# Optimization experiments

Hardware: AMD Instinct MI355X
Metric: run time of the kernel (lower is better)

## Reference

```python
import jax, jax.numpy as jnp
import numpy as np

B, T, S, H, K, NQ = 16, 512, 320, 512, 1024, 4


def setup_inputs() -> dict:
    key = jax.random.key(0)
    ks = jax.random.split(key, 16)
    inp = {
        "waveform": jax.random.normal(ks[0], (B, T * S), dtype=jnp.float32) * 0.1,
        # Encoder: Linear(S->H) + LayerNorm(H)
        "enc_w": jax.random.normal(ks[1], (S, H), dtype=jnp.float32) * 0.02,
        "enc_b": jnp.zeros((H,), dtype=jnp.float32),
        "ln_g": jnp.ones((H,), dtype=jnp.float32),
        "ln_b": jnp.zeros((H,), dtype=jnp.float32),
        # Residual VQ codebooks: (NQ, K, H)
        "codebooks": jax.random.normal(ks[2], (NQ, K, H), dtype=jnp.float32) * 0.5,
        # 2-layer LSTM (torch gate order i,f,g,o), stacked over layers
        "lstm_wi": jax.random.normal(ks[3], (2, 4 * H, H), dtype=jnp.float32) * 0.04,
        "lstm_wh": jax.random.normal(ks[4], (2, 4 * H, H), dtype=jnp.float32) * 0.04,
        "lstm_bi": jnp.zeros((2, 4 * H), dtype=jnp.float32),
        "lstm_bh": jnp.zeros((2, 4 * H), dtype=jnp.float32),
        # Decoder out projection: Linear(H->S)
        "dec_w": jax.random.normal(ks[5], (H, S), dtype=jnp.float32) * 0.02,
        "dec_b": jnp.zeros((S,), dtype=jnp.float32),
    }
    return inp


def _layer_norm(x, g, b, eps=1e-5):
    mu = jnp.mean(x, axis=-1, keepdims=True)
    var = jnp.mean((x - mu) ** 2, axis=-1, keepdims=True)
    return (x - mu) * jax.lax.rsqrt(var + eps) * g + b


def _lstm_layer(x, wi, wh, bi, bh):
    # x: (B, T, H) -> (B, T, H); torch gate order i, f, g, o
    h0 = jnp.zeros((x.shape[0], wh.shape[1]), dtype=x.dtype)
    c0 = jnp.zeros_like(h0)

    def step(carry, xt):
        h, c = carry
        gates = xt @ wi.T + h @ wh.T + bi + bh  # (B, 4H)
        i, f, g, o = jnp.split(gates, 4, axis=-1)
        c = jax.nn.sigmoid(f) * c + jax.nn.sigmoid(i) * jnp.tanh(g)
        h = jax.nn.sigmoid(o) * jnp.tanh(c)
        return (h, c), h

    _, ys = jax.lax.scan(step, (h0, c0), x.transpose(1, 0, 2))
    return ys.transpose(1, 0, 2)


def reference(waveform, enc_w, enc_b, ln_g, ln_b, codebooks,
              lstm_wi, lstm_wh, lstm_bi, lstm_bh, dec_w, dec_b):
    # Encoder: unflatten to frames, project, LayerNorm, ReLU -> (B, T, H)
    x = waveform.reshape(B, T, S) @ enc_w + enc_b
    x = jax.nn.relu(_layer_norm(x, ln_g, ln_b))

    # Residual VQ (encodec-style): nearest-neighbor + straight-through estimator
    residual = x
    quant_out = jnp.zeros_like(x)
    losses = []
    for q in range(NQ):
        E = codebooks[q]  # (K, H)
        # squared L2 distance: ||r||^2 - 2 r.E^T + ||E||^2  -> (B, T, K)
        d = (jnp.sum(residual ** 2, axis=-1, keepdims=True)
             - 2.0 * jnp.einsum("bth,kh->btk", residual, E)
             + jnp.sum(E ** 2, axis=-1))
        idx = jnp.argmin(d, axis=-1)  # (B, T)
        quantized = E[idx]  # (B, T, H)
        losses.append(jnp.mean((jax.lax.stop_gradient(quantized) - residual) ** 2))
        q_st = residual + jax.lax.stop_gradient(quantized - residual)  # STE
        quant_out = quant_out + q_st
        residual = residual - q_st
    codebook_loss = jnp.stack(losses)  # (NQ,)

    # Decoder: 2-layer LSTM + out projection, flatten frames back to samples
    h = _lstm_layer(quant_out, lstm_wi[0], lstm_wh[0], lstm_bi[0], lstm_bh[0])
    h = _lstm_layer(h, lstm_wi[1], lstm_wh[1], lstm_bi[1], lstm_bh[1])
    out = h @ dec_w + dec_b  # (B, T, S)
    recon = out.reshape(B, T * S)
    return recon, codebook_loss
```

## Files before the change

### kernel.cpp

```cpp
#include <hip/hip_runtime.h>
#include <cmath>


template<bool BT>
__global__ __launch_bounds__(256)
void gemm64(const float* __restrict__ A, const float* __restrict__ B,
            float* __restrict__ C, int M, int N, int K,
            const float* __restrict__ bias1, const float* __restrict__ bias2)
{
    __shared__ float Al[32][68];
    __shared__ float Bl[32][68];
    const int m0 = blockIdx.y * 64, n0 = blockIdx.x * 64;
    const int t = threadIdx.x;
    const int tm = t >> 4, tn = t & 15;
    float acc[4][4] = {{0.f, 0.f, 0.f, 0.f}};

    for (int k0 = 0; k0 < K; k0 += 32) {
        #pragma unroll
        for (int i = 0; i < 2; i++) {
            int f4 = t + i * 256;
            int row = f4 >> 3, c4 = f4 & 7;
            float4 v = *(const float4*)(A + (size_t)(m0 + row) * K + k0 + c4 * 4);
            Al[c4*4+0][row] = v.x; Al[c4*4+1][row] = v.y;
            Al[c4*4+2][row] = v.z; Al[c4*4+3][row] = v.w;
        }
        if (BT) {
            #pragma unroll
            for (int i = 0; i < 2; i++) {
                int f4 = t + i * 256;
                int row = f4 >> 3, c4 = f4 & 7;
                float4 v = *(const float4*)(B + (size_t)(n0 + row) * K + k0 + c4 * 4);
                Bl[c4*4+0][row] = v.x; Bl[c4*4+1][row] = v.y;
                Bl[c4*4+2][row] = v.z; Bl[c4*4+3][row] = v.w;
            }
        } else {
            #pragma unroll
            for (int i = 0; i < 2; i++) {
                int f4 = t + i * 256;
                int kk = f4 >> 4, c4 = f4 & 15;
                float4 v = *(const float4*)(B + (size_t)(k0 + kk) * N + n0 + c4 * 4);
                *(float4*)&Bl[kk][c4 * 4] = v;
            }
        }
        __syncthreads();
        #pragma unroll
        for (int k = 0; k < 32; k++) {
            float4 a4 = *(const float4*)&Al[k][tm * 4];
            float4 b4 = *(const float4*)&Bl[k][tn * 4];
            float av[4] = {a4.x, a4.y, a4.z, a4.w};
            float bv[4] = {b4.x, b4.y, b4.z, b4.w};
            #pragma unroll
            for (int i = 0; i < 4; i++)
                #pragma unroll
                for (int j = 0; j < 4; j++)
                    acc[i][j] = fmaf(av[i], bv[j], acc[i][j]);
        }
        __syncthreads();
    }
    float bn[4];
    #pragma unroll
    for (int j = 0; j < 4; j++) {
        float bb = 0.f;
        if (bias1) bb += bias1[n0 + tn * 4 + j];
        if (bias2) bb += bias2[n0 + tn * 4 + j];
        bn[j] = bb;
    }
    #pragma unroll
    for (int i = 0; i < 4; i++) {
        float4 o;
        o.x = acc[i][0] + bn[0]; o.y = acc[i][1] + bn[1];
        o.z = acc[i][2] + bn[2]; o.w = acc[i][3] + bn[3];
        *(float4*)(C + (size_t)(m0 + tm * 4 + i) * N + n0 + tn * 4) = o;
    }
}

template<bool BT>
__global__ __launch_bounds__(256)
void gemm128(const float* __restrict__ A, const float* __restrict__ B,
             float* __restrict__ C, int M, int N, int K,
             const float* __restrict__ bias1, const float* __restrict__ bias2)
{
    __shared__ float Al[16][132];
    __shared__ float Bl[16][132];
    const int m0 = blockIdx.y * 128, n0 = blockIdx.x * 128;
    const int t = threadIdx.x;
    const int tm = t >> 4, tn = t & 15;
    float acc[8][8] = {};

    for (int k0 = 0; k0 < K; k0 += 16) {
        #pragma unroll
        for (int i = 0; i < 2; i++) {
            int f4 = t + i * 256;
            int row = f4 >> 2, c4 = f4 & 3;
            float4 v = *(const float4*)(A + (size_t)(m0 + row) * K + k0 + c4 * 4);
            Al[c4*4+0][row] = v.x; Al[c4*4+1][row] = v.y;
            Al[c4*4+2][row] = v.z; Al[c4*4+3][row] = v.w;
        }
        if (BT) {
            #pragma unroll
            for (int i = 0; i < 2; i++) {
                int f4 = t + i * 256;
                int row = f4 >> 2, c4 = f4 & 3;
                float4 v = *(const float4*)(B + (size_t)(n0 + row) * K + k0 + c4 * 4);
                Bl[c4*4+0][row] = v.x; Bl[c4*4+1][row] = v.y;
                Bl[c4*4+2][row] = v.z; Bl[c4*4+3][row] = v.w;
            }
        } else {
            #pragma unroll
            for (int i = 0; i < 2; i++) {
                int f4 = t + i * 256;
                int kk = f4 >> 5, c4 = f4 & 31;
                float4 v = *(const float4*)(B + (size_t)(k0 + kk) * N + n0 + c4 * 4);
                *(float4*)&Bl[kk][c4 * 4] = v;
            }
        }
        __syncthreads();
        #pragma unroll
        for (int k = 0; k < 16; k++) {
            float4 a0 = *(const float4*)&Al[k][tm * 8];
            float4 a1 = *(const float4*)&Al[k][tm * 8 + 4];
            float4 b0 = *(const float4*)&Bl[k][tn * 8];
            float4 b1 = *(const float4*)&Bl[k][tn * 8 + 4];
            float av[8] = {a0.x,a0.y,a0.z,a0.w,a1.x,a1.y,a1.z,a1.w};
            float bv[8] = {b0.x,b0.y,b0.z,b0.w,b1.x,b1.y,b1.z,b1.w};
            #pragma unroll
            for (int i = 0; i < 8; i++)
                #pragma unroll
                for (int j = 0; j < 8; j++)
                    acc[i][j] = fmaf(av[i], bv[j], acc[i][j]);
        }
        __syncthreads();
    }
    float bn[8];
    #pragma unroll
    for (int j = 0; j < 8; j++) {
        float bb = 0.f;
        if (bias1) bb += bias1[n0 + tn * 8 + j];
        if (bias2) bb += bias2[n0 + tn * 8 + j];
        bn[j] = bb;
    }
    #pragma unroll
    for (int i = 0; i < 8; i++) {
        float* cp = C + (size_t)(m0 + tm * 8 + i) * N + n0 + tn * 8;
        float4 o0, o1;
        o0.x = acc[i][0]+bn[0]; o0.y = acc[i][1]+bn[1];
        o0.z = acc[i][2]+bn[2]; o0.w = acc[i][3]+bn[3];
        o1.x = acc[i][4]+bn[4]; o1.y = acc[i][5]+bn[5];
        o1.z = acc[i][6]+bn[6]; o1.w = acc[i][7]+bn[7];
        *(float4*)cp = o0;
        *(float4*)(cp + 4) = o1;
    }
}

__global__ __launch_bounds__(256)
void ln_relu_kernel(float* __restrict__ X, const float* __restrict__ g,
                    const float* __restrict__ bb)
{
    __shared__ float red[256];
    __shared__ float stat[2];
    const int row = blockIdx.x, t = threadIdx.x;
    float x0 = X[(size_t)row * 512 + t];
    float x1 = X[(size_t)row * 512 + 256 + t];
    red[t] = x0 + x1;
    __syncthreads();
    for (int o = 128; o > 0; o >>= 1) { if (t < o) red[t] += red[t + o]; __syncthreads(); }
    if (t == 0) stat[0] = red[0] * (1.f / 512.f);
    __syncthreads();
    float mu = stat[0];
    float d0 = x0 - mu, d1 = x1 - mu;
    red[t] = d0 * d0 + d1 * d1;
    __syncthreads();
    for (int o = 128; o > 0; o >>= 1) { if (t < o) red[t] += red[t + o]; __syncthreads(); }
    if (t == 0) stat[1] = red[0] * (1.f / 512.f);
    __syncthreads();
    float rs = rsqrtf(stat[1] + 1e-5f);
    float y0 = d0 * rs * g[t] + bb[t];
    float y1 = d1 * rs * g[256 + t] + bb[256 + t];
    X[(size_t)row * 512 + t] = fmaxf(y0, 0.f);
    X[(size_t)row * 512 + 256 + t] = fmaxf(y1, 0.f);
}

__global__ __launch_bounds__(256)
void rownorm_kernel(const float* __restrict__ Ein, float* __restrict__ norms)
{
    __shared__ float red[256];
    const int row = blockIdx.x, t = threadIdx.x;
    float a = Ein[(size_t)row * 512 + t];
    float b = Ein[(size_t)row * 512 + 256 + t];
    red[t] = a * a + b * b;
    __syncthreads();
    for (int o = 128; o > 0; o >>= 1) { if (t < o) red[t] += red[t + o]; __syncthreads(); }
    if (t == 0) norms[row] = red[0];
}

__global__ __launch_bounds__(256)
void vq_update_kernel(const float* __restrict__ D, const float* __restrict__ norms,
                      const float* __restrict__ cb, float* __restrict__ residual,
                      float* __restrict__ quant, float* __restrict__ loss_acc,
                      int first)
{
    __shared__ unsigned long long red[256];
    __shared__ float fred[256];
    __shared__ int sidx;
    __shared__ float sdmin;
    const int tok = blockIdx.x, t = threadIdx.x;
    unsigned long long best = ~0ull;
    #pragma unroll
    for (int i = 0; i < 4; i++) {
        int k = t + i * 256;
        float d = fmaf(-2.f, D[(size_t)tok * 1024 + k], norms[k]);
        unsigned u = __float_as_uint(d);
        u = (u & 0x80000000u) ? ~u : (u | 0x80000000u);
        unsigned long long p = ((unsigned long long)u << 32) | (unsigned)k;
        best = p < best ? p : best;
    }
    red[t] = best;
    __syncthreads();
    for (int o = 128; o > 0; o >>= 1) {
        if (t < o) red[t] = red[t + o] < red[t] ? red[t + o] : red[t];
        __syncthreads();
    }
    if (t == 0) {
        unsigned long long r0 = red[0];
        sidx = (int)(r0 & 0xffffffffu);
        unsigned uv = (unsigned)(r0 >> 32);
        unsigned orig = (uv & 0x80000000u) ? (uv ^ 0x80000000u) : ~uv;
        sdmin = __uint_as_float(orig);
    }
    float r0v = residual[(size_t)tok * 512 + t];
    float r1v = residual[(size_t)tok * 512 + 256 + t];
    fred[t] = r0v * r0v + r1v * r1v;
    __syncthreads();
    for (int o = 128; o > 0; o >>= 1) { if (t < o) fred[t] += fred[t + o]; __syncthreads(); }
    int idx = sidx;
    if (t == 0) atomicAdd(loss_acc, sdmin + fred[0]);
    const float* E = cb + (size_t)idx * 512;
    float e0 = E[t], e1 = E[256 + t];
    float q0 = r0v + (e0 - r0v);
    float q1 = r1v + (e1 - r1v);
    residual[(size_t)tok * 512 + t]       = r0v - q0;
    residual[(size_t)tok * 512 + 256 + t] = r1v - q1;
    const int tokP = ((tok & 511) << 4) | (tok >> 9);
    if (first) {
        quant[(size_t)tokP * 512 + t]       = q0;
        quant[(size_t)tokP * 512 + 256 + t] = q1;
    } else {
        quant[(size_t)tokP * 512 + t]       += q0;
        quant[(size_t)tokP * 512 + 256 + t] += q1;
    }
}


#define LSTRIDE 137
#define SLOT_STRIDE 16
#define PART_SK 271

__device__ __forceinline__ int sw(int blk) { return (blk & 7) * 17 + (blk >> 3); }

__device__ __forceinline__ void wait_vm0() {
    asm volatile("s_waitcnt vmcnt(0)" ::: "memory");
}

__device__ __forceinline__ void ld4_issue(float4& a, float4& b, float4& c, float4& d,
                                          const float4* p0, const float4* p1,
                                          const float4* p2, const float4* p3)
{
    asm volatile(
        "global_load_dwordx4 %0, %4, off sc0 sc1\n\t"
        "global_load_dwordx4 %1, %5, off sc0 sc1\n\t"
        "global_load_dwordx4 %2, %6, off sc0 sc1\n\t"
        "global_load_dwordx4 %3, %7, off sc0 sc1"
        : "=&v"(a), "=&v"(b), "=&v"(c), "=&v"(d)
        : "v"(p0), "v"(p1), "v"(p2), "v"(p3)
        : "memory");
}

__device__ __forceinline__ void stage8t(float4* d4, const float* src, int t)
{
    const float4* s4 = (const float4*)src;
    float4 v[8];
    ld4_issue(v[0], v[1], v[2], v[3], s4 + t, s4 + t + 256, s4 + t + 512, s4 + t + 768);
    ld4_issue(v[4], v[5], v[6], v[7], s4 + t + 1024, s4 + t + 1280, s4 + t + 1536, s4 + t + 1792);
    wait_vm0();
    #pragma unroll
    for (int i = 0; i < 8; i++) {
        int G = t + i * 256;
        int b = G & 15, blk = G >> 4;
        d4[b * LSTRIDE + sw(blk)] = v[i];
    }
}

__device__ __forceinline__ void stage16t(float4* d1, const float* src1,
                                         float4* d2, const float* src2, int t)
{
    const float4* s1 = (const float4*)src1;
    const float4* s2 = (const float4*)src2;
    float4 v[16];
    ld4_issue(v[0], v[1], v[2], v[3],  s1 + t, s1 + t + 256, s1 + t + 512, s1 + t + 768);
    ld4_issue(v[4], v[5], v[6], v[7],  s1 + t + 1024, s1 + t + 1280, s1 + t + 1536, s1 + t + 1792);
    ld4_issue(v[8], v[9], v[10],v[11], s2 + t, s2 + t + 256, s2 + t + 512, s2 + t + 768);
    ld4_issue(v[12],v[13],v[14],v[15], s2 + t + 1024, s2 + t + 1280, s2 + t + 1536, s2 + t + 1792);
    wait_vm0();
    #pragma unroll
    for (int i = 0; i < 8; i++) {
        int G = t + i * 256;
        int b = G & 15, blk = G >> 4;
        int idx = b * LSTRIDE + sw(blk);
        d1[idx] = v[i];
        d2[idx] = v[i + 8];
    }
}

__device__ __forceinline__ unsigned slot_load(const unsigned* p)
{
    return __hip_atomic_load(p, __ATOMIC_RELAXED, __HIP_MEMORY_SCOPE_AGENT);
}

__device__ __forceinline__ void poll128(const unsigned* slots, int lane, unsigned tgt)
{
    const unsigned* p0 = slots + (size_t)lane * SLOT_STRIDE;
    const unsigned* p1 = slots + (size_t)(64 + lane) * SLOT_STRIDE;
    int spins = 0;
    while (true) {
        unsigned a = slot_load(p0);
        unsigned b = slot_load(p1);
        if (__all(a >= tgt && b >= tgt)) break;
        __builtin_amdgcn_s_sleep(2);
        if (++spins > 300000) break;
    }
}

__global__ __launch_bounds__(256, 1)
void lstm_fused_kernel(const float* __restrict__ P1,
                       const float* __restrict__ wh1,
                       const float* __restrict__ wi2,
                       const float* __restrict__ wh2,
                       const float* __restrict__ bi2,
                       const float* __restrict__ bh2,
                       float* __restrict__ H2out,
                       float* __restrict__ h1hist,
                       float* __restrict__ h2hist,
                       unsigned* __restrict__ slots)
{
    __shared__ float4 hl4[16 * LSTRIDE];
    __shared__ float4 hl24[16 * LSTRIDE];
    __shared__ float part[32 * PART_SK];
    __shared__ float gl[256];
    __shared__ float c_lds[64];

    const int t = threadIdx.x;
    const int role = blockIdx.x >> 7;
    const int bid = blockIdx.x & 127;
    const int ks = t >> 3;
    const int q  = t & 7;
    const int c0 = q * 2;
    const int j_base = bid * 4;
    const int cl_r = t >> 4, b_r = t & 15;
    const int gate_r = cl_r >> 2, jj_r = cl_r & 3;
    const int w = t >> 6, lane = t & 63;

    unsigned* slots0 = slots;
    unsigned* slots1 = slots + 128 * SLOT_STRIDE;

    float wh0[16], wh1r[16], wx0[16], wx1[16];
    {
        const float* whp = (role == 0) ? wh1 : wh2;
        const int gate0 = c0 >> 2, jj0 = c0 & 3;
        const float* wr = whp + (size_t)(gate0 * 512 + j_base + jj0) * 512 + ks * 16;
        #pragma unroll
        for (int i = 0; i < 16; i++) { wh0[i] = wr[i]; wh1r[i] = wr[512 + i]; }
    }
    if (role == 1) {
        const int gate0 = c0 >> 2, jj0 = c0 & 3;
        const float* wr = wi2 + (size_t)(gate0 * 512 + j_base + jj0) * 512 + ks * 16;
        #pragma unroll
        for (int i = 0; i < 16; i++) { wx0[i] = wr[i]; wx1[i] = wr[512 + i]; }
    } else {
        #pragma unroll
        for (int i = 0; i < 16; i++) { wx0[i] = 0.f; wx1[i] = 0.f; }
    }
    float bias2v = 0.f;
    if (role == 1) {
        int col = gate_r * 512 + j_base + jj_r;
        bias2v = bi2[col] + bh2[col];
    }
    if (t < 64) c_lds[t] = 0.f;

    if (role == 0) {
        const float* pvp = P1 + (size_t)b_r * 2048 + gate_r * 512 + j_base + jj_r;
        float pv = pvp[0];
        for (int s = 0; s < 512; s++) {
            if (w == 0) poll128(slots0, lane, (unsigned)s);
            __syncthreads();
            if (s > 0) {
                stage8t(hl4, h1hist + (size_t)(s - 1) * 8192, t);
            } else {
                float4 z = make_float4(0.f, 0.f, 0.f, 0.f);
                #pragma unroll
                for (int i = 0; i < 9; i++) {
                    int idx = t + i * 256;
                    if (idx < 16 * LSTRIDE) hl4[idx] = z;
                }
            }
            float pv_next = (s < 511) ? pvp[(size_t)(s + 1) * 32768] : 0.f;
            __syncthreads();
            float acc0[16], acc1[16];
            #pragma unroll
            for (int b = 0; b < 16; b++) { acc0[b] = 0.f; acc1[b] = 0.f; }
            #pragma unroll
            for (int b = 0; b < 16; b++) {
                const float4* hrow = hl4 + b * LSTRIDE;
                #pragma unroll
                for (int j4 = 0; j4 < 4; j4++) {
                    float4 h4 = hrow[sw(ks * 4 + j4)];
                    acc0[b] = fmaf(h4.x, wh0[j4*4+0], acc0[b]);
                    acc1[b] = fmaf(h4.x, wh1r[j4*4+0], acc1[b]);
                    acc0[b] = fmaf(h4.y, wh0[j4*4+1], acc0[b]);
                    acc1[b] = fmaf(h4.y, wh1r[j4*4+1], acc1[b]);
                    acc0[b] = fmaf(h4.z, wh0[j4*4+2], acc0[b]);
                    acc1[b] = fmaf(h4.z, wh1r[j4*4+2], acc1[b]);
                    acc0[b] = fmaf(h4.w, wh0[j4*4+3], acc0[b]);
                    acc1[b] = fmaf(h4.w, wh1r[j4*4+3], acc1[b]);
                }
            }
            #pragma unroll
            for (int b = 0; b < 16; b++) {
                part[ks * PART_SK + c0 * 17 + b]       = acc0[b];
                part[ks * PART_SK + (c0 + 1) * 17 + b] = acc1[b];
            }
            __syncthreads();
            float gv = pv;
            #pragma unroll
            for (int k = 0; k < 32; k++)
                gv += part[k * PART_SK + cl_r * 17 + b_r];
            gl[cl_r * 16 + b_r] = gv;
            __syncthreads();
            if (t < 64) {
                int b = t >> 2, jr = t & 3;
                float iv = gl[(0 + jr) * 16 + b];
                float fv = gl[(4 + jr) * 16 + b];
                float gg = gl[(8 + jr) * 16 + b];
                float ov = gl[(12 + jr) * 16 + b];
                float ig = 1.f / (1.f + expf(-iv));
                float fg = 1.f / (1.f + expf(-fv));
                float og = 1.f / (1.f + expf(-ov));
                float cn = fg * c_lds[t] + ig * tanhf(gg);
                float hn = og * tanhf(cn);
                c_lds[t] = cn;
                __hip_atomic_store(&h1hist[(size_t)s * 8192 + bid * 64 + t], hn,
                                   __ATOMIC_RELAXED, __HIP_MEMORY_SCOPE_AGENT);
            }
            wait_vm0();
            if (t == 0)
                __hip_atomic_store(&slots0[bid * SLOT_STRIDE], (unsigned)(s + 1),
                                   __ATOMIC_RELAXED, __HIP_MEMORY_SCOPE_AGENT);
            pv = pv_next;
        }
    } else {
        for (int m = 0; m < 512; m++) {
            if (w == 0)      poll128(slots0, lane, (unsigned)(m + 1));
            else if (w == 1) poll128(slots1, lane, (unsigned)m);
            __syncthreads();
            if (m > 0) {
                stage16t(hl4, h1hist + (size_t)m * 8192,
                         hl24, h2hist + (size_t)(m - 1) * 8192, t);
            } else {
                stage8t(hl4, h1hist, t);
                float4 z = make_float4(0.f, 0.f, 0.f, 0.f);
                #pragma unroll
                for (int i = 0; i < 9; i++) {
                    int idx = t + i * 256;
                    if (idx < 16 * LSTRIDE) hl24[idx] = z;
                }
            }
            __syncthreads();
            float acc0[16], acc1[16];
            #pragma unroll
            for (int b = 0; b < 16; b++) { acc0[b] = 0.f; acc1[b] = 0.f; }
            #pragma unroll
            for (int b = 0; b < 16; b++) {
                const float4* xrow = hl4 + b * LSTRIDE;
                const float4* hrow = hl24 + b * LSTRIDE;
                #pragma unroll
                for (int j4 = 0; j4 < 4; j4++) {
                    float4 x4 = xrow[sw(ks * 4 + j4)];
                    acc0[b] = fmaf(x4.x, wx0[j4*4+0], acc0[b]);
                    acc1[b] = fmaf(x4.x, wx1[j4*4+0], acc1[b]);
                    acc0[b] = fmaf(x4.y, wx0[j4*4+1], acc0[b]);
                    acc1[b] = fmaf(x4.y, wx1[j4*4+1], acc1[b]);
                    acc0[b] = fmaf(x4.z, wx0[j4*4+2], acc0[b]);
                    acc1[b] = fmaf(x4.z, wx1[j4*4+2], acc1[b]);
                    acc0[b] = fmaf(x4.w, wx0[j4*4+3], acc0[b]);
                    acc1[b] = fmaf(x4.w, wx1[j4*4+3], acc1[b]);
                }
                #pragma unroll
                for (int j4 = 0; j4 < 4; j4++) {
                    float4 h4 = hrow[sw(ks * 4 + j4)];
                    acc0[b] = fmaf(h4.x, wh0[j4*4+0], acc0[b]);
                    acc1[b] = fmaf(h4.x, wh1r[j4*4+0], acc1[b]);
                    acc0[b] = fmaf(h4.y, wh0[j4*4+1], acc0[b]);
                    acc1[b] = fmaf(h4.y, wh1r[j4*4+1], acc1[b]);
                    acc0[b] = fmaf(h4.z, wh0[j4*4+2], acc0[b]);
                    acc1[b] = fmaf(h4.z, wh1r[j4*4+2], acc1[b]);
                    acc0[b] = fmaf(h4.w, wh0[j4*4+3], acc0[b]);
                    acc1[b] = fmaf(h4.w, wh1r[j4*4+3], acc1[b]);
                }
            }
            #pragma unroll
            for (int b = 0; b < 16; b++) {
                part[ks * PART_SK + c0 * 17 + b]       = acc0[b];
                part[ks * PART_SK + (c0 + 1) * 17 + b] = acc1[b];
            }
            __syncthreads();
            float gv = bias2v;
            #pragma unroll
            for (int k = 0; k < 32; k++)
                gv += part[k * PART_SK + cl_r * 17 + b_r];
            gl[cl_r * 16 + b_r] = gv;
            __syncthreads();
            if (t < 64) {
                int b = t >> 2, jr = t & 3;
                float iv = gl[(0 + jr) * 16 + b];
                float fv = gl[(4 + jr) * 16 + b];
                float gg = gl[(8 + jr) * 16 + b];
                float ov = gl[(12 + jr) * 16 + b];
                float ig = 1.f / (1.f + expf(-iv));
                float fg = 1.f / (1.f + expf(-fv));
                float og = 1.f / (1.f + expf(-ov));
                float cn = fg * c_lds[t] + ig * tanhf(gg);
                float hn = og * tanhf(cn);
                c_lds[t] = cn;
                int j = j_base + jr;
                __hip_atomic_store(&h2hist[(size_t)m * 8192 + bid * 64 + t], hn,
                                   __ATOMIC_RELAXED, __HIP_MEMORY_SCOPE_AGENT);
                H2out[(size_t)(b * 512 + m) * 512 + j] = hn;
            }
            wait_vm0();
            if (t == 0)
                __hip_atomic_store(&slots1[bid * SLOT_STRIDE], (unsigned)(m + 1),
                                   __ATOMIC_RELAXED, __HIP_MEMORY_SCOPE_AGENT);
        }
    }
}

__global__ void finalize_loss_kernel(const float* __restrict__ acc, float* __restrict__ out)
{
    int q = threadIdx.x;
    if (q < 4) out[2621440 + q] = acc[q] * (1.f / 4194304.f);
}

extern "C" void kernel_launch(void* const* d_in, const int* in_sizes, int n_in,
                              void* d_out, int out_size, void* d_ws, size_t ws_size,
                              hipStream_t stream)
{
    const float* waveform  = (const float*)d_in[0];
    const float* enc_w     = (const float*)d_in[1];
    const float* enc_b     = (const float*)d_in[2];
    const float* ln_g      = (const float*)d_in[3];
    const float* ln_b      = (const float*)d_in[4];
    const float* codebooks = (const float*)d_in[5];
    const float* lstm_wi   = (const float*)d_in[6];
    const float* lstm_wh   = (const float*)d_in[7];
    const float* lstm_bi   = (const float*)d_in[8];
    const float* lstm_bh   = (const float*)d_in[9];
    const float* dec_w     = (const float*)d_in[10];
    const float* dec_b     = (const float*)d_in[11];
    float* out = (float*)d_out;

    float* ws = (float*)d_ws;
    float* residual = ws;
    float* quant    = ws + 4194304;
    float* H2       = ws + 8388608;
    float* big      = ws + 12582912;
    unsigned* slots = (unsigned*)(ws + 29360128);
    float* norms    = ws + 29392896;
    float* loss_acc = ws + 29396992;

    hipMemsetAsync(loss_acc, 0, 16 * sizeof(float), stream);
    hipMemsetAsync(slots, 0, 4096 * sizeof(unsigned), stream);

    gemm128<false><<<dim3(4, 64), 256, 0, stream>>>(waveform, enc_w, residual,
                                                    8192, 512, 320, enc_b, nullptr);
    ln_relu_kernel<<<8192, 256, 0, stream>>>(residual, ln_g, ln_b);

    rownorm_kernel<<<4096, 256, 0, stream>>>(codebooks, norms);
    for (int q = 0; q < 4; q++) {
        const float* cb = codebooks + (size_t)q * 1024 * 512;
        gemm128<true><<<dim3(8, 64), 256, 0, stream>>>(residual, cb, big,
                                                       8192, 1024, 512, nullptr, nullptr);
        vq_update_kernel<<<8192, 256, 0, stream>>>(big, norms + q * 1024, cb,
                                                   residual, quant, loss_acc + q, q == 0);
    }

    gemm128<true><<<dim3(16, 64), 256, 0, stream>>>(quant, lstm_wi, big,
                                                    8192, 2048, 512, lstm_bi, lstm_bh);
    lstm_fused_kernel<<<dim3(256), dim3(256), 0, stream>>>(
        big, lstm_wh, lstm_wi + (size_t)2048 * 512, lstm_wh + (size_t)2048 * 512,
        lstm_bi + 2048, lstm_bh + 2048, H2, quant, residual, slots);

    gemm64<false><<<dim3(5, 128), 256, 0, stream>>>(H2, dec_w, out,
                                                    8192, 320, 512, dec_b, nullptr);
    finalize_loss_kernel<<<1, 4, 0, stream>>>(loss_acc, out);
}
```

Before: 4.469 ms.

## Fuse VQ distance argmin into codebook GEMM epilogue and simplify LSTM gate reduction

Adds a gemm_vq kernel that computes distances and a per-tile packed (distance, index) minimum in its epilogue, writing 8 candidates per token instead of the full 8192x1024 distance matrix. vq_update then only reduces those 8 candidates, which removes a large write and read of the distance buffer in each of the four quantizer stages. The LSTM kernel also drops the gl staging buffer and one barrier per step: the 64 active threads now reduce all four gates directly from the partial sums, with the input projections and biases loaded per gate. The trade-off is more serial reduction work per thread inside the recurrent step.

```diff
diff --git a/kernel.cpp b/kernel.cpp
--- a/kernel.cpp
+++ b/kernel.cpp
@@ -153,6 +153,80 @@
 }
 
 __global__ __launch_bounds__(256)
+void gemm_vq(const float* __restrict__ A, const float* __restrict__ B,
+             const float* __restrict__ norms, unsigned long long* __restrict__ pairs,
+             int M, int N, int K)
+{
+    __shared__ float Al[16][132];
+    __shared__ float Bl[16][132];
+    __shared__ unsigned long long redvq[128][17];
+    const int m0 = blockIdx.y * 128, n0 = blockIdx.x * 128;
+    const int t = threadIdx.x;
+    const int tm = t >> 4, tn = t & 15;
+    float acc[8][8] = {};
+
+    for (int k0 = 0; k0 < K; k0 += 16) {
+        #pragma unroll
+        for (int i = 0; i < 2; i++) {
+            int f4 = t + i * 256;
+            int row = f4 >> 2, c4 = f4 & 3;
+            float4 v = *(const float4*)(A + (size_t)(m0 + row) * K + k0 + c4 * 4);
+            Al[c4*4+0][row] = v.x; Al[c4*4+1][row] = v.y;
+            Al[c4*4+2][row] = v.z; Al[c4*4+3][row] = v.w;
+        }
+        #pragma unroll
+        for (int i = 0; i < 2; i++) {
+            int f4 = t + i * 256;
+            int row = f4 >> 2, c4 = f4 & 3;
+            float4 v = *(const float4*)(B + (size_t)(n0 + row) * K + k0 + c4 * 4);
+            Bl[c4*4+0][row] = v.x; Bl[c4*4+1][row] = v.y;
+            Bl[c4*4+2][row] = v.z; Bl[c4*4+3][row] = v.w;
+        }
+        __syncthreads();
+        #pragma unroll
+        for (int k = 0; k < 16; k++) {
+            float4 a0 = *(const float4*)&Al[k][tm * 8];
+            float4 a1 = *(const float4*)&Al[k][tm * 8 + 4];
+            float4 b0 = *(const float4*)&Bl[k][tn * 8];
+            float4 b1 = *(const float4*)&Bl[k][tn * 8 + 4];
+            float av[8] = {a0.x,a0.y,a0.z,a0.w,a1.x,a1.y,a1.z,a1.w};
+            float bv[8] = {b0.x,b0.y,b0.z,b0.w,b1.x,b1.y,b1.z,b1.w};
+            #pragma unroll
+            for (int i = 0; i < 8; i++)
+                #pragma unroll
+                for (int j = 0; j < 8; j++)
+                    acc[i][j] = fmaf(av[i], bv[j], acc[i][j]);
+        }
+        __syncthreads();
+    }
+    unsigned long long best[8];
+    #pragma unroll
+    for (int i = 0; i < 8; i++) best[i] = ~0ull;
+    #pragma unroll
+    for (int j = 0; j < 8; j++) {
+        int col = n0 + tn * 8 + j;
+        float nj = norms[col];
+        #pragma unroll
+        for (int i = 0; i < 8; i++) {
+            float d = fmaf(-2.f, acc[i][j], nj);
+            unsigned u = __float_as_uint(d);
+            u = (u & 0x80000000u) ? ~u : (u | 0x80000000u);
+            unsigned long long p = ((unsigned long long)u << 32) | (unsigned)col;
+            best[i] = p < best[i] ? p : best[i];
+        }
+    }
+    #pragma unroll
+    for (int i = 0; i < 8; i++) redvq[tm * 8 + i][tn] = best[i];
+    __syncthreads();
+    if (t < 128) {
+        unsigned long long m = redvq[t][0];
+        #pragma unroll
+        for (int e = 1; e < 16; e++) m = redvq[t][e] < m ? redvq[t][e] : m;
+        pairs[(size_t)(m0 + t) * 8 + blockIdx.x] = m;
+    }
+}
+
+__global__ __launch_bounds__(256)
 void ln_relu_kernel(float* __restrict__ X, const float* __restrict__ g,
                     const float* __restrict__ bb)
 {
@@ -194,7 +268,7 @@
 }
 
 __global__ __launch_bounds__(256)
-void vq_update_kernel(const float* __restrict__ D, const float* __restrict__ norms,
+void vq_update_kernel(const unsigned long long* __restrict__ pairs,
                       const float* __restrict__ cb, float* __restrict__ residual,
                       float* __restrict__ quant, float* __restrict__ loss_acc,
                       int first)
@@ -205,15 +279,7 @@
     __shared__ float sdmin;
     const int tok = blockIdx.x, t = threadIdx.x;
     unsigned long long best = ~0ull;
-    #pragma unroll
-    for (int i = 0; i < 4; i++) {
-        int k = t + i * 256;
-        float d = fmaf(-2.f, D[(size_t)tok * 1024 + k], norms[k]);
-        unsigned u = __float_as_uint(d);
-        u = (u & 0x80000000u) ? ~u : (u | 0x80000000u);
-        unsigned long long p = ((unsigned long long)u << 32) | (unsigned)k;
-        best = p < best ? p : best;
-    }
+    if (t < 8) best = pairs[(size_t)tok * 8 + t];
     red[t] = best;
     __syncthreads();
     for (int o = 128; o > 0; o >>= 1) {
@@ -253,7 +319,6 @@
 
 #define LSTRIDE 137
 #define SLOT_STRIDE 16
-#define PART_SK 271
 
 __device__ __forceinline__ int sw(int blk) { return (blk & 7) * 17 + (blk >> 3); }
 
@@ -344,8 +409,7 @@
 {
     __shared__ float4 hl4[16 * LSTRIDE];
     __shared__ float4 hl24[16 * LSTRIDE];
-    __shared__ float part[32 * PART_SK];
-    __shared__ float gl[256];
+    __shared__ float part[32 * 271];
     __shared__ float c_lds[64];
 
     const int t = threadIdx.x;
@@ -355,8 +419,6 @@
     const int q  = t & 7;
     const int c0 = q * 2;
     const int j_base = bid * 4;
-    const int cl_r = t >> 4, b_r = t & 15;
-    const int gate_r = cl_r >> 2, jj_r = cl_r & 3;
     const int w = t >> 6, lane = t & 63;
 
     unsigned* slots0 = slots;
@@ -379,16 +441,22 @@
         #pragma unroll
         for (int i = 0; i < 16; i++) { wx0[i] = 0.f; wx1[i] = 0.f; }
     }
-    float bias2v = 0.f;
-    if (role == 1) {
-        int col = gate_r * 512 + j_base + jj_r;
-        bias2v = bi2[col] + bh2[col];
+    float bias4[4] = {0.f, 0.f, 0.f, 0.f};
+    if (role == 1 && t < 64) {
+        int col0 = j_base + (t & 3);
+        #pragma unroll
+        for (int g = 0; g < 4; g++)
+            bias4[g] = bi2[g * 512 + col0] + bh2[g * 512 + col0];
     }
     if (t < 64) c_lds[t] = 0.f;
+    __syncthreads();
 
     if (role == 0) {
-        const float* pvp = P1 + (size_t)b_r * 2048 + gate_r * 512 + j_base + jj_r;
-        float pv = pvp[0];
+        const float* pvp = P1 + (size_t)(t >> 2) * 2048 + j_base + (t & 3);
+        float pv4[4] = {0.f, 0.f, 0.f, 0.f};
+        if (t < 64) {
+            pv4[0] = pvp[0]; pv4[1] = pvp[512]; pv4[2] = pvp[1024]; pv4[3] = pvp[1536];
+        }
         for (int s = 0; s < 512; s++) {
             if (w == 0) poll128(slots0, lane, (unsigned)s);
             __syncthreads();
@@ -402,7 +470,11 @@
                     if (idx < 16 * LSTRIDE) hl4[idx] = z;
                 }
             }
-            float pv_next = (s < 511) ? pvp[(size_t)(s + 1) * 32768] : 0.f;
+            float pv4n[4] = {0.f, 0.f, 0.f, 0.f};
+            if (t < 64 && s < 511) {
+                const float* pn = pvp + (size_t)(s + 1) * 32768;
+                pv4n[0] = pn[0]; pv4n[1] = pn[512]; pv4n[2] = pn[1024]; pv4n[3] = pn[1536];
+            }
             __syncthreads();
             float acc0[16], acc1[16];
             #pragma unroll
@@ -425,26 +497,25 @@
             }
             #pragma unroll
             for (int b = 0; b < 16; b++) {
-                part[ks * PART_SK + c0 * 17 + b]       = acc0[b];
-                part[ks * PART_SK + (c0 + 1) * 17 + b] = acc1[b];
-            }
-            __syncthreads();
-            float gv = pv;
-            #pragma unroll
-            for (int k = 0; k < 32; k++)
-                gv += part[k * PART_SK + cl_r * 17 + b_r];
-            gl[cl_r * 16 + b_r] = gv;
+                part[ks * 271 + c0 * 17 + b]       = acc0[b];
+                part[ks * 271 + (c0 + 1) * 17 + b] = acc1[b];
+            }
             __syncthreads();
             if (t < 64) {
                 int b = t >> 2, jr = t & 3;
-                float iv = gl[(0 + jr) * 16 + b];
-                float fv = gl[(4 + jr) * 16 + b];
-                float gg = gl[(8 + jr) * 16 + b];
-                float ov = gl[(12 + jr) * 16 + b];
-                float ig = 1.f / (1.f + expf(-iv));
-                float fg = 1.f / (1.f + expf(-fv));
-                float og = 1.f / (1.f + expf(-ov));
-                float cn = fg * c_lds[t] + ig * tanhf(gg);
+                float gv0 = pv4[0], gv1 = pv4[1], gv2 = pv4[2], gv3 = pv4[3];
+                #pragma unroll
+                for (int k = 0; k < 32; k++) {
+                    const float* pk = &part[k * 271 + jr * 17 + b];
+                    gv0 += pk[0];
+                    gv1 += pk[68];
+                    gv2 += pk[136];
+                    gv3 += pk[204];
+                }
+                float ig = 1.f / (1.f + expf(-gv0));
+                float fg = 1.f / (1.f + expf(-gv1));
+                float og = 1.f / (1.f + expf(-gv3));
+                float cn = fg * c_lds[t] + ig * tanhf(gv2);
                 float hn = og * tanhf(cn);
                 c_lds[t] = cn;
                 __hip_atomic_store(&h1hist[(size_t)s * 8192 + bid * 64 + t], hn,
@@ -454,7 +525,7 @@
             if (t == 0)
                 __hip_atomic_store(&slots0[bid * SLOT_STRIDE], (unsigned)(s + 1),
                                    __ATOMIC_RELAXED, __HIP_MEMORY_SCOPE_AGENT);
-            pv = pv_next;
+            pv4[0] = pv4n[0]; pv4[1] = pv4n[1]; pv4[2] = pv4n[2]; pv4[3] = pv4n[3];
         }
     } else {
         for (int m = 0; m < 512; m++) {
@@ -508,26 +579,25 @@
             }
             #pragma unroll
             for (int b = 0; b < 16; b++) {
-                part[ks * PART_SK + c0 * 17 + b]       = acc0[b];
-                part[ks * PART_SK + (c0 + 1) * 17 + b] = acc1[b];
-            }
-            __syncthreads();
-            float gv = bias2v;
-            #pragma unroll
-            for (int k = 0; k < 32; k++)
-                gv += part[k * PART_SK + cl_r * 17 + b_r];
-            gl[cl_r * 16 + b_r] = gv;
+                part[ks * 271 + c0 * 17 + b]       = acc0[b];
+                part[ks * 271 + (c0 + 1) * 17 + b] = acc1[b];
+            }
             __syncthreads();
             if (t < 64) {
                 int b = t >> 2, jr = t & 3;
-                float iv = gl[(0 + jr) * 16 + b];
-                float fv = gl[(4 + jr) * 16 + b];
-                float gg = gl[(8 + jr) * 16 + b];
-                float ov = gl[(12 + jr) * 16 + b];
-                float ig = 1.f / (1.f + expf(-iv));
-                float fg = 1.f / (1.f + expf(-fv));
-                float og = 1.f / (1.f + expf(-ov));
-                float cn = fg * c_lds[t] + ig * tanhf(gg);
+                float gv0 = bias4[0], gv1 = bias4[1], gv2 = bias4[2], gv3 = bias4[3];
+                #pragma unroll
+                for (int k = 0; k < 32; k++) {
+                    const float* pk = &part[k * 271 + jr * 17 + b];
+                    gv0 += pk[0];
+                    gv1 += pk[68];
+                    gv2 += pk[136];
+                    gv3 += pk[204];
+                }
+                float ig = 1.f / (1.f + expf(-gv0));
+                float fg = 1.f / (1.f + expf(-gv1));
+                float og = 1.f / (1.f + expf(-gv3));
+                float cn = fg * c_lds[t] + ig * tanhf(gv2);
                 float hn = og * tanhf(cn);
                 c_lds[t] = cn;
                 int j = j_base + jr;
@@ -572,6 +642,7 @@
     float* quant    = ws + 4194304;
     float* H2       = ws + 8388608;
     float* big      = ws + 12582912;
+    unsigned long long* pairs = (unsigned long long*)(ws + 12582912);
     unsigned* slots = (unsigned*)(ws + 29360128);
     float* norms    = ws + 29392896;
     float* loss_acc = ws + 29396992;
@@ -586,10 +657,10 @@
     rownorm_kernel<<<4096, 256, 0, stream>>>(codebooks, norms);
     for (int q = 0; q < 4; q++) {
         const float* cb = codebooks + (size_t)q * 1024 * 512;
-        gemm128<true><<<dim3(8, 64), 256, 0, stream>>>(residual, cb, big,
-                                                       8192, 1024, 512, nullptr, nullptr);
-        vq_update_kernel<<<8192, 256, 0, stream>>>(big, norms + q * 1024, cb,
-                                                   residual, quant, loss_acc + q, q == 0);
+        gemm_vq<<<dim3(8, 64), 256, 0, stream>>>(residual, cb, norms + q * 1024,
+                                                 pairs, 8192, 1024, 512);
+        vq_update_kernel<<<8192, 256, 0, stream>>>(pairs, cb, residual, quant,
+                                                   loss_acc + q, q == 0);
     }
 
     gemm128<true><<<dim3(16, 64), 256, 0, stream>>>(quant, lstm_wi, big,
```

Result: slower. 4.666 ms (+4.4%).

## Fuse VQ distance epilogue and partial argmin into codebook GEMM

Applied to the files above, without the earlier changes.

Replaces the codebook-distance GEMM that wrote a full 8192x1024 distance matrix with a GEMM whose epilogue computes norm-adjusted distances and a per-block packed (distance,index) minimum. Each row gets 8 partial minima, which the update kernel reduces instead of scanning 1024 distances. This cuts the large intermediate write and read per quantizer stage, at the cost of an extra shared-memory reduction in the GEMM epilogue.

```diff
diff --git a/kernel.cpp b/kernel.cpp
--- a/kernel.cpp
+++ b/kernel.cpp
@@ -153,6 +153,82 @@
 }
 
 __global__ __launch_bounds__(256)
+void gemm_vq(const float* __restrict__ A, const float* __restrict__ B,
+             const float* __restrict__ norms, unsigned long long* __restrict__ pairs,
+             int M, int N, int K)
+{
+    __shared__ unsigned long long smem_u64[2176];
+    float (*Al)[132] = (float(*)[132])smem_u64;
+    float (*Bl)[132] = (float(*)[132])((float*)smem_u64 + 16 * 132);
+    unsigned long long (*redvq)[17] = (unsigned long long(*)[17])smem_u64;
+
+    const int m0 = blockIdx.y * 128, n0 = blockIdx.x * 128;
+    const int t = threadIdx.x;
+    const int tm = t >> 4, tn = t & 15;
+    float acc[8][8] = {};
+
+    for (int k0 = 0; k0 < K; k0 += 16) {
+        #pragma unroll
+        for (int i = 0; i < 2; i++) {
+            int f4 = t + i * 256;
+            int row = f4 >> 2, c4 = f4 & 3;
+            float4 v = *(const float4*)(A + (size_t)(m0 + row) * K + k0 + c4 * 4);
+            Al[c4*4+0][row] = v.x; Al[c4*4+1][row] = v.y;
+            Al[c4*4+2][row] = v.z; Al[c4*4+3][row] = v.w;
+        }
+        #pragma unroll
+        for (int i = 0; i < 2; i++) {
+            int f4 = t + i * 256;
+            int row = f4 >> 2, c4 = f4 & 3;
+            float4 v = *(const float4*)(B + (size_t)(n0 + row) * K + k0 + c4 * 4);
+            Bl[c4*4+0][row] = v.x; Bl[c4*4+1][row] = v.y;
+            Bl[c4*4+2][row] = v.z; Bl[c4*4+3][row] = v.w;
+        }
+        __syncthreads();
+        #pragma unroll
+        for (int k = 0; k < 16; k++) {
+            float4 a0 = *(const float4*)&Al[k][tm * 8];
+            float4 a1 = *(const float4*)&Al[k][tm * 8 + 4];
+            float4 b0 = *(const float4*)&Bl[k][tn * 8];
+            float4 b1 = *(const float4*)&Bl[k][tn * 8 + 4];
+            float av[8] = {a0.x,a0.y,a0.z,a0.w,a1.x,a1.y,a1.z,a1.w};
+            float bv[8] = {b0.x,b0.y,b0.z,b0.w,b1.x,b1.y,b1.z,b1.w};
+            #pragma unroll
+            for (int i = 0; i < 8; i++)
+                #pragma unroll
+                for (int j = 0; j < 8; j++)
+                    acc[i][j] = fmaf(av[i], bv[j], acc[i][j]);
+        }
+        __syncthreads();
+    }
+    unsigned long long best[8];
+    #pragma unroll
+    for (int i = 0; i < 8; i++) best[i] = ~0ull;
+    #pragma unroll
+    for (int j = 0; j < 8; j++) {
+        int col = n0 + tn * 8 + j;
+        float nj = norms[col];
+        #pragma unroll
+        for (int i = 0; i < 8; i++) {
+            float d = fmaf(-2.f, acc[i][j], nj);
+            unsigned u = __float_as_uint(d);
+            u = (u & 0x80000000u) ? ~u : (u | 0x80000000u);
+            unsigned long long p = ((unsigned long long)u << 32) | (unsigned)col;
+            best[i] = p < best[i] ? p : best[i];
+        }
+    }
+    #pragma unroll
+    for (int i = 0; i < 8; i++) redvq[tm * 8 + i][tn] = best[i];
+    __syncthreads();
+    if (t < 128) {
+        unsigned long long m = redvq[t][0];
+        #pragma unroll
+        for (int e = 1; e < 16; e++) m = redvq[t][e] < m ? redvq[t][e] : m;
+        pairs[(size_t)(m0 + t) * 8 + blockIdx.x] = m;
+    }
+}
+
+__global__ __launch_bounds__(256)
 void ln_relu_kernel(float* __restrict__ X, const float* __restrict__ g,
                     const float* __restrict__ bb)
 {
@@ -194,7 +270,7 @@
 }
 
 __global__ __launch_bounds__(256)
-void vq_update_kernel(const float* __restrict__ D, const float* __restrict__ norms,
+void vq_update_kernel(const unsigned long long* __restrict__ pairs,
                       const float* __restrict__ cb, float* __restrict__ residual,
                       float* __restrict__ quant, float* __restrict__ loss_acc,
                       int first)
@@ -205,15 +281,7 @@
     __shared__ float sdmin;
     const int tok = blockIdx.x, t = threadIdx.x;
     unsigned long long best = ~0ull;
-    #pragma unroll
-    for (int i = 0; i < 4; i++) {
-        int k = t + i * 256;
-        float d = fmaf(-2.f, D[(size_t)tok * 1024 + k], norms[k]);
-        unsigned u = __float_as_uint(d);
-        u = (u & 0x80000000u) ? ~u : (u | 0x80000000u);
-        unsigned long long p = ((unsigned long long)u << 32) | (unsigned)k;
-        best = p < best ? p : best;
-    }
+    if (t < 8) best = pairs[(size_t)tok * 8 + t];
     red[t] = best;
     __syncthreads();
     for (int o = 128; o > 0; o >>= 1) {
@@ -572,6 +640,7 @@
     float* quant    = ws + 4194304;
     float* H2       = ws + 8388608;
     float* big      = ws + 12582912;
+    unsigned long long* pairs = (unsigned long long*)(ws + 12582912);
     unsigned* slots = (unsigned*)(ws + 29360128);
     float* norms    = ws + 29392896;
     float* loss_acc = ws + 29396992;
@@ -586,10 +655,10 @@
     rownorm_kernel<<<4096, 256, 0, stream>>>(codebooks, norms);
     for (int q = 0; q < 4; q++) {
         const float* cb = codebooks + (size_t)q * 1024 * 512;
-        gemm128<true><<<dim3(8, 64), 256, 0, stream>>>(residual, cb, big,
-                                                       8192, 1024, 512, nullptr, nullptr);
-        vq_update_kernel<<<8192, 256, 0, stream>>>(big, norms + q * 1024, cb,
-                                                   residual, quant, loss_acc + q, q == 0);
+        gemm_vq<<<dim3(8, 64), 256, 0, stream>>>(residual, cb, norms + q * 1024,
+                                                 pairs, 8192, 1024, 512);
+        vq_update_kernel<<<8192, 256, 0, stream>>>(pairs, cb, residual, quant,
+                                                   loss_acc + q, q == 0);
     }
 
     gemm128<true><<<dim3(16, 64), 256, 0, stream>>>(quant, lstm_wi, big,
```

Result: no change. 4.537 ms (+1.5%).
